# Kernel optimization log

Hardware: AMD Instinct MI355X
Metric: run time of the kernel (lower is better)

## Reference

```python
import jax, jax.numpy as jnp
import numpy as np
import math

# ---- HashGridEncoder constants (from init_kwargs) ----
L = 16            # levels
LOG2T = 19
T = 1 << LOG2T    # hash table size per level
F = 2             # features per entry
N_MIN = 16
N_MAX = 2048
N_PTS = 524288    # number of query points
BB_MIN = np.zeros(3, np.float32)
BB_MAX = np.ones(3, np.float32)
B = math.exp((math.log(N_MAX) - math.log(N_MIN)) / (L - 1))
RES = np.array([math.floor(N_MIN * B ** i) for i in range(L)], dtype=np.float32)  # per-level grid resolution
VERTS = np.array([[0,0,0],[0,0,1],[0,1,0],[0,1,1],[1,0,0],[1,0,1],[1,1,0],[1,1,1]], dtype=np.int32)  # 8 cube corners
PI = np.array([1, 2654435761, 805459861], dtype=np.uint32)  # spatial hash primes
MASK = np.uint32((1 << 19) - 1)  # hard-coded mask from source


def setup_inputs() -> dict:
    key = jax.random.key(0)
    k1, k2 = jax.random.split(key)
    xyz = jax.random.uniform(k1, (N_PTS, 3), dtype=jnp.float32)  # points inside bbox [0,1]^3
    # nn.init.uniform_(weight, -1e-4, 1e-4)
    tables = jax.random.uniform(k2, (L, T, F), minval=-1e-4, maxval=1e-4, dtype=jnp.float32)
    return {"xyz": xyz, "tables": tables}


def reference(xyz, tables):
    # cell size per level: (bb_max - bb_min) / resolution  -> [L,3]
    cell = (BB_MAX - BB_MIN)[None, :] / RES[:, None]
    # normalized grid coords for all levels at once: [L,N,3]
    u = (xyz[None, :, :] - BB_MIN) / cell[:, None, :]
    mi = jnp.floor(u).astype(jnp.int32)            # min corner index [L,N,3]
    d = u - mi.astype(jnp.float32)                 # trilinear fracs == (xyz - min_vertex)/cell, [L,N,3]
    # 8 corner integer coords: [L,N,8,3]; uint32 wrapping matches int64-mul + low-19-bit mask
    corners = (mi[:, :, None, :] + VERTS[None, None]).astype(jnp.uint32)
    h = (corners[..., 0] * PI[0]) ^ (corners[..., 1] * PI[1]) ^ (corners[..., 2] * PI[2])
    h = (h & MASK).astype(jnp.int32)               # hash indices [L,N,8], all < T
    # gather all levels in one flat lookup
    flat = tables.reshape(L * T, F)
    idx = h + (jnp.arange(L, dtype=jnp.int32) * T)[:, None, None]
    emb = flat[idx]                                # [L,N,8,F]
    # trilinear weights: prod over axes of d (corner bit 1) or 1-d (corner bit 0) -> [L,N,8]
    w = jnp.prod(jnp.where(VERTS[None, None].astype(bool), d[:, :, None, :], 1.0 - d[:, :, None, :]), axis=-1)
    c = jnp.einsum('lnv,lnvf->lnf', w, emb)        # interpolated features [L,N,F]
    # torch.cat(embedded, dim=-1): level-major concat -> [N, L*F]
    return jnp.moveaxis(c, 0, 1).reshape(xyz.shape[0], L * F)
```

## Files before the change

### kernel.cpp

```cpp
#include <hip/hip_runtime.h>
#include <cmath>

#define NLEVELS 16
#define HMASK   0x7FFFFu
#define NPTS    524288
#define NBUCKET 32768

typedef float v4f __attribute__((ext_vector_type(4)));
typedef float v2f __attribute__((ext_vector_type(2)));
typedef _Float16 h2 __attribute__((ext_vector_type(2)));

struct LevelParams {
    float cell[NLEVELS];
};

__device__ __forceinline__ unsigned spread5(unsigned v) {
    return (v & 1u) | ((v & 2u) << 2) | ((v & 4u) << 4) |
           ((v & 8u) << 6) | ((v & 16u) << 8);
}

__device__ __forceinline__ unsigned morton_key(float x, float y, float z) {
    unsigned bx = min(31u, (unsigned)(x * 32.0f));
    unsigned by = min(31u, (unsigned)(y * 32.0f));
    unsigned bz = min(31u, (unsigned)(z * 32.0f));
    return spread5(bx) | (spread5(by) << 1) | (spread5(bz) << 2);
}

__device__ __forceinline__ void ngp_hash(
    float x, float y, float z, float cell, unsigned* __restrict__ h,
    float& dx, float& dy, float& dz, unsigned& ix_out)
{
    const float ux = x / cell;
    const float uy = y / cell;
    const float uz = z / cell;
    const float fx = floorf(ux);
    const float fy = floorf(uy);
    const float fz = floorf(uz);
    dx = ux - fx;
    dy = uy - fy;
    dz = uz - fz;

    const unsigned ix = (unsigned)(int)fx;
    const unsigned iy = (unsigned)(int)fy;
    const unsigned iz = (unsigned)(int)fz;
    ix_out = ix;

    const unsigned hx0 = ix;
    const unsigned hx1 = ix + 1u;
    const unsigned hy0 = iy * 2654435761u;
    const unsigned hy1 = (iy + 1u) * 2654435761u;
    const unsigned hz0 = iz * 805459861u;
    const unsigned hz1 = (iz + 1u) * 805459861u;

    h[0] = (hx0 ^ hy0 ^ hz0) & HMASK;
    h[1] = (hx0 ^ hy0 ^ hz1) & HMASK;
    h[2] = (hx0 ^ hy1 ^ hz0) & HMASK;
    h[3] = (hx0 ^ hy1 ^ hz1) & HMASK;
    h[4] = (hx1 ^ hy0 ^ hz0) & HMASK;
    h[5] = (hx1 ^ hy0 ^ hz1) & HMASK;
    h[6] = (hx1 ^ hy1 ^ hz0) & HMASK;
    h[7] = (hx1 ^ hy1 ^ hz1) & HMASK;
}

__device__ __forceinline__ void ngp_weights(
    float dx, float dy, float dz, float* __restrict__ w)
{
    const float wx0 = 1.0f - dx;
    const float wy0 = 1.0f - dy;
    const float wz0 = 1.0f - dz;
    const float p00 = wx0 * wy0;
    const float p01 = wx0 * dy;
    const float p10 = dx * wy0;
    const float p11 = dx * dy;
    w[0] = p00 * wz0;
    w[1] = p00 * dz;
    w[2] = p01 * wz0;
    w[3] = p01 * dz;
    w[4] = p10 * wz0;
    w[5] = p10 * dz;
    w[6] = p11 * wz0;
    w[7] = p11 * dz;
}

__device__ __forceinline__ v2f ngp_combine(
    const float* __restrict__ w, const v2f* __restrict__ e)
{
    float c0 = w[0] * e[0].x;
    float c1 = w[0] * e[0].y;
    #pragma unroll
    for (int c = 1; c < 8; ++c) {
        c0 += w[c] * e[c].x;
        c1 += w[c] * e[c].y;
    }
    v2f r = { c0, c1 };
    return r;
}

__global__ __launch_bounds__(256) void bucket_count(
    const float* __restrict__ xyz, unsigned* __restrict__ counts)
{
    const int n = blockIdx.x * 256 + threadIdx.x;
    const float x = xyz[3 * n + 0];
    const float y = xyz[3 * n + 1];
    const float z = xyz[3 * n + 2];
    atomicAdd(&counts[morton_key(x, y, z)], 1u);
}

__global__ __launch_bounds__(1024) void bucket_scan(
    const unsigned* __restrict__ counts, unsigned* __restrict__ cursor)
{
    __shared__ unsigned c[NBUCKET];
    __shared__ unsigned wsum[16];
    const unsigned t = threadIdx.x;
    const unsigned lane = t & 63u;
    const unsigned wid = t >> 6;

    #pragma unroll
    for (int i = 0; i < 32; ++i) {
        const unsigned idx = (unsigned)i * 1024u + t;
        c[idx ^ ((idx >> 5) & 31u)] = counts[idx];
    }
    __syncthreads();

    unsigned s = 0;
    #pragma unroll
    for (int i = 0; i < 32; ++i) {
        const unsigned idx = t * 32u + (unsigned)i;
        s += c[idx ^ ((idx >> 5) & 31u)];
    }

    unsigned v = s;
    #pragma unroll
    for (unsigned off = 1; off < 64; off <<= 1) {
        const unsigned u = __shfl_up(v, off);
        if (lane >= off) v += u;
    }
    if (lane == 63u) wsum[wid] = v;
    __syncthreads();

    unsigned woff = 0;
    #pragma unroll
    for (unsigned w = 0; w < 16; ++w)
        woff += (w < wid) ? wsum[w] : 0u;

    unsigned excl = woff + (v - s);
    #pragma unroll
    for (int i = 0; i < 32; ++i) {
        const unsigned idx = t * 32u + (unsigned)i;
        const unsigned sw  = idx ^ ((idx >> 5) & 31u);
        const unsigned tmp = c[sw];
        c[sw] = excl;
        excl += tmp;
    }
    __syncthreads();

    #pragma unroll
    for (int i = 0; i < 32; ++i) {
        const unsigned idx = (unsigned)i * 1024u + t;
        cursor[idx] = c[idx ^ ((idx >> 5) & 31u)];
    }
}

__global__ __launch_bounds__(256) void bucket_scatter(
    const float* __restrict__ xyz, unsigned* __restrict__ cursor,
    v4f* __restrict__ pts)
{
    const int n = blockIdx.x * 256 + threadIdx.x;
    const float x = xyz[3 * n + 0];
    const float y = xyz[3 * n + 1];
    const float z = xyz[3 * n + 2];
    const unsigned key = morton_key(x, y, z);
    const unsigned p = atomicAdd(&cursor[key], 1u);
    v4f v = { x, y, z, __uint_as_float((unsigned)n) };
    __builtin_nontemporal_store(v, &pts[p]);
}

__global__ __launch_bounds__(256) void ngp_phase1(
    const v4f* __restrict__ pts,
    const float* __restrict__ tables,
    h2* __restrict__ ws,
    LevelParams lp)
{
    const unsigned b = blockIdx.x;
    const int level = (int)(b >> 11);
    const int chunk = (int)(b & 2047u);
    const int p = chunk * 256 + threadIdx.x;

    const v4f q = pts[p];

    const float cell = lp.cell[level];
    const v2f* __restrict__ tab = (const v2f*)tables + ((size_t)level << 19);

    unsigned h[8];
    float dx, dy, dz;
    unsigned ix;
    ngp_hash(q.x, q.y, q.z, cell, h, dx, dy, dz, ix);

    v2f e[8];
    if (!(ix & 1u)) {
        if (level >= 5) {
            v4f p0, p1, p2, p3;
            const v4f* a0 = (const v4f*)(tab + (h[0] & ~1u));
            const v4f* a1 = (const v4f*)(tab + (h[1] & ~1u));
            const v4f* a2 = (const v4f*)(tab + (h[2] & ~1u));
            const v4f* a3 = (const v4f*)(tab + (h[3] & ~1u));
            asm volatile(
                "global_load_dwordx4 %0, %4, off sc0\n\t"
                "global_load_dwordx4 %1, %5, off sc0\n\t"
                "global_load_dwordx4 %2, %6, off sc0\n\t"
                "global_load_dwordx4 %3, %7, off sc0"
                : "=&v"(p0), "=&v"(p1), "=&v"(p2), "=&v"(p3)
                : "v"(a0), "v"(a1), "v"(a2), "v"(a3));
            asm volatile(
                "s_waitcnt vmcnt(0)"
                : "+v"(p0), "+v"(p1), "+v"(p2), "+v"(p3));
            const bool o0 = (h[0] & 1u) != 0u;
            const bool o1 = (h[1] & 1u) != 0u;
            const bool o2 = (h[2] & 1u) != 0u;
            const bool o3 = (h[3] & 1u) != 0u;
            e[0].x = o0 ? p0.z : p0.x;  e[0].y = o0 ? p0.w : p0.y;
            e[4].x = o0 ? p0.x : p0.z;  e[4].y = o0 ? p0.y : p0.w;
            e[1].x = o1 ? p1.z : p1.x;  e[1].y = o1 ? p1.w : p1.y;
            e[5].x = o1 ? p1.x : p1.z;  e[5].y = o1 ? p1.y : p1.w;
            e[2].x = o2 ? p2.z : p2.x;  e[2].y = o2 ? p2.w : p2.y;
            e[6].x = o2 ? p2.x : p2.z;  e[6].y = o2 ? p2.y : p2.w;
            e[3].x = o3 ? p3.z : p3.x;  e[3].y = o3 ? p3.w : p3.y;
            e[7].x = o3 ? p3.x : p3.z;  e[7].y = o3 ? p3.y : p3.w;
        } else {
            #pragma unroll
            for (int c = 0; c < 4; ++c) {
                const v4f pv = *(const v4f*)(tab + (h[c] & ~1u));
                const bool o = (h[c] & 1u) != 0u;
                e[c].x     = o ? pv.z : pv.x;  e[c].y     = o ? pv.w : pv.y;
                e[c + 4].x = o ? pv.x : pv.z;  e[c + 4].y = o ? pv.y : pv.w;
            }
        }
    } else {
        if (level >= 5) {
            v2f e0, e1, e2, e3, e4, e5, e6, e7;
            asm volatile(
                "global_load_dwordx2 %0, %8, off sc0\n\t"
                "global_load_dwordx2 %1, %9, off sc0\n\t"
                "global_load_dwordx2 %2, %10, off sc0\n\t"
                "global_load_dwordx2 %3, %11, off sc0\n\t"
                "global_load_dwordx2 %4, %12, off sc0\n\t"
                "global_load_dwordx2 %5, %13, off sc0\n\t"
                "global_load_dwordx2 %6, %14, off sc0\n\t"
                "global_load_dwordx2 %7, %15, off sc0"
                : "=&v"(e0), "=&v"(e1), "=&v"(e2), "=&v"(e3),
                  "=&v"(e4), "=&v"(e5), "=&v"(e6), "=&v"(e7)
                : "v"(tab + h[0]), "v"(tab + h[1]), "v"(tab + h[2]), "v"(tab + h[3]),
                  "v"(tab + h[4]), "v"(tab + h[5]), "v"(tab + h[6]), "v"(tab + h[7]));
            asm volatile(
                "s_waitcnt vmcnt(0)"
                : "+v"(e0), "+v"(e1), "+v"(e2), "+v"(e3),
                  "+v"(e4), "+v"(e5), "+v"(e6), "+v"(e7));
            e[0] = e0; e[1] = e1; e[2] = e2; e[3] = e3;
            e[4] = e4; e[5] = e5; e[6] = e6; e[7] = e7;
        } else {
            #pragma unroll
            for (int c = 0; c < 8; ++c) e[c] = tab[h[c]];
        }
    }

    float w[8];
    ngp_weights(dx, dy, dz, w);

    const v2f r2 = ngp_combine(w, e);

    h2 hv = { (_Float16)r2.x, (_Float16)r2.y };
    __builtin_nontemporal_store(hv, &ws[(size_t)level * NPTS + p]);
}

#define P2S 258

__global__ __launch_bounds__(256) void ngp_phase2(
    const h2* __restrict__ ws,
    const v4f* __restrict__ pts,
    float* __restrict__ out)
{
    __shared__ h2 lds[NLEVELS * P2S];
    __shared__ unsigned nperm[256];
    const unsigned base = blockIdx.x * 256;
    const unsigned t = threadIdx.x;

    nperm[t] = __float_as_uint(pts[base + t].w);
    #pragma unroll
    for (int l = 0; l < NLEVELS; ++l)
        lds[l * P2S + t] =
            __builtin_nontemporal_load(&ws[(size_t)l * NPTS + base + t]);

    __syncthreads();

    #pragma unroll
    for (int it = 0; it < 8; ++it) {
        const unsigned j = it * 256 + t;
        const unsigned pl = j >> 3;
        const unsigned k = j & 7u;
        const h2 a = lds[(2u * k)      * P2S + pl];
        const h2 b = lds[(2u * k + 1u) * P2S + pl];
        v4f v = { (float)a.x, (float)a.y, (float)b.x, (float)b.y };
        __builtin_nontemporal_store(
            v, (v4f*)(out + (size_t)nperm[pl] * 32 + k * 4));
    }
}

__global__ __launch_bounds__(256) void ngp_encode(
    const float* __restrict__ xyz,
    const float* __restrict__ tables,
    float* __restrict__ out,
    LevelParams lp)
{
    const int n = blockIdx.x * 256 + threadIdx.x;
    const float x = xyz[3 * n + 0];
    const float y = xyz[3 * n + 1];
    const float z = xyz[3 * n + 2];

    float acc[2 * NLEVELS];
    const v2f* __restrict__ tab_base = (const v2f*)tables;

    #pragma unroll
    for (int l = 0; l < NLEVELS; ++l) {
        unsigned h[8];
        float dx, dy, dz;
        unsigned ix;
        ngp_hash(x, y, z, lp.cell[l], h, dx, dy, dz, ix);
        const v2f* __restrict__ tab = tab_base + ((size_t)l << 19);
        v2f e[8];
        #pragma unroll
        for (int c = 0; c < 8; ++c) e[c] = tab[h[c]];
        float w[8];
        ngp_weights(dx, dy, dz, w);
        const v2f r = ngp_combine(w, e);
        acc[2 * l + 0] = r.x;
        acc[2 * l + 1] = r.y;
    }

    v4f* o4 = (v4f*)(out + (size_t)n * 32);
    #pragma unroll
    for (int j = 0; j < 8; ++j) {
        v4f v = { acc[4 * j + 0], acc[4 * j + 1],
                  acc[4 * j + 2], acc[4 * j + 3] };
        o4[j] = v;
    }
}

extern "C" void kernel_launch(void* const* d_in, const int* in_sizes, int n_in,
                              void* d_out, int out_size, void* d_ws, size_t ws_size,
                              hipStream_t stream) {
    const float* xyz    = (const float*)d_in[0];
    const float* tables = (const float*)d_in[1];
    float* out          = (float*)d_out;

    LevelParams lp;
    const double B = std::exp((std::log(2048.0) - std::log(16.0)) / 15.0);
    for (int i = 0; i < NLEVELS; ++i) {
        const double r = std::floor(16.0 * std::pow(B, (double)i));
        lp.cell[i] = 1.0f / (float)r;
    }

    const size_t off_feat   = 0;
    const size_t off_pts    = off_feat + (size_t)NLEVELS * NPTS * sizeof(h2);
    const size_t off_counts = off_pts + (size_t)NPTS * sizeof(v4f);
    const size_t off_cursor = off_counts + (size_t)NBUCKET * sizeof(unsigned);
    const size_t ws_needed  = off_cursor + (size_t)NBUCKET * sizeof(unsigned);

    if (ws_size >= ws_needed) {
        char* wsb = (char*)d_ws;
        h2*       ws_feat = (h2*)(wsb + off_feat);
        v4f*      pts     = (v4f*)(wsb + off_pts);
        unsigned* counts  = (unsigned*)(wsb + off_counts);
        unsigned* cursor  = (unsigned*)(wsb + off_cursor);

        hipMemsetAsync(counts, 0, NBUCKET * sizeof(unsigned), stream);
        hipLaunchKernelGGL(bucket_count, dim3(NPTS / 256), dim3(256), 0, stream,
                           xyz, counts);
        hipLaunchKernelGGL(bucket_scan, dim3(1), dim3(1024), 0, stream,
                           counts, cursor);
        hipLaunchKernelGGL(bucket_scatter, dim3(NPTS / 256), dim3(256), 0, stream,
                           xyz, cursor, pts);
        hipLaunchKernelGGL(ngp_phase1, dim3(NLEVELS * (NPTS / 256)), dim3(256), 0, stream,
                           pts, tables, ws_feat, lp);
        hipLaunchKernelGGL(ngp_phase2, dim3(NPTS / 256), dim3(256), 0, stream,
                           ws_feat, pts, out);
    } else {
        hipLaunchKernelGGL(ngp_encode, dim3(NPTS / 256), dim3(256), 0, stream,
                           xyz, tables, out, lp);
    }
}
```

Baseline: 324.2 us.

## Replace single-block bucket scan with two-pass multi-block scan

The 32768-bucket exclusive prefix scan ran in a single 1024-thread block. It is now split into two kernels across 128 blocks. The first computes per-block totals, and the second has each block reduce the preceding block totals and then do an in-block scan. This aims to remove the serial single-CU scan step from the pipeline, at the cost of one extra kernel launch and a small extra workspace buffer.

```diff
diff --git a/kernel.cpp b/kernel.cpp
--- a/kernel.cpp
+++ b/kernel.cpp
@@ -106,59 +106,53 @@
     atomicAdd(&counts[morton_key(x, y, z)], 1u);
 }
 
-__global__ __launch_bounds__(1024) void bucket_scan(
-    const unsigned* __restrict__ counts, unsigned* __restrict__ cursor)
-{
-    __shared__ unsigned c[NBUCKET];
-    __shared__ unsigned wsum[16];
+__global__ __launch_bounds__(256) void scan_pre(
+    const unsigned* __restrict__ counts, unsigned* __restrict__ btot)
+{
+    __shared__ unsigned ws4[4];
+    const unsigned j = blockIdx.x;
+    const unsigned t = threadIdx.x;
+    unsigned v = counts[j * 256u + t];
+    #pragma unroll
+    for (unsigned off = 1; off < 64; off <<= 1) v += __shfl_xor(v, off);
+    if ((t & 63u) == 0u) ws4[t >> 6] = v;
+    __syncthreads();
+    if (t == 0u) btot[j] = ws4[0] + ws4[1] + ws4[2] + ws4[3];
+}
+
+__global__ __launch_bounds__(256) void scan_main(
+    const unsigned* __restrict__ counts, const unsigned* __restrict__ btot,
+    unsigned* __restrict__ cursor)
+{
+    __shared__ unsigned bsum4[4];
+    __shared__ unsigned wsum4[4];
+    const unsigned j = blockIdx.x;
     const unsigned t = threadIdx.x;
     const unsigned lane = t & 63u;
     const unsigned wid = t >> 6;
 
-    #pragma unroll
-    for (int i = 0; i < 32; ++i) {
-        const unsigned idx = (unsigned)i * 1024u + t;
-        c[idx ^ ((idx >> 5) & 31u)] = counts[idx];
-    }
+    unsigned bv = (t < j) ? btot[t] : 0u;
+    #pragma unroll
+    for (unsigned off = 1; off < 64; off <<= 1) bv += __shfl_xor(bv, off);
+    if (lane == 0u) bsum4[wid] = bv;
     __syncthreads();
-
-    unsigned s = 0;
-    #pragma unroll
-    for (int i = 0; i < 32; ++i) {
-        const unsigned idx = t * 32u + (unsigned)i;
-        s += c[idx ^ ((idx >> 5) & 31u)];
-    }
-
-    unsigned v = s;
+    const unsigned base = bsum4[0] + bsum4[1] + bsum4[2] + bsum4[3];
+
+    const unsigned idx = j * 256u + t;
+    const unsigned v = counts[idx];
+    unsigned incl = v;
     #pragma unroll
     for (unsigned off = 1; off < 64; off <<= 1) {
-        const unsigned u = __shfl_up(v, off);
-        if (lane >= off) v += u;
-    }
-    if (lane == 63u) wsum[wid] = v;
+        const unsigned u = __shfl_up(incl, off);
+        if (lane >= off) incl += u;
+    }
+    if (lane == 63u) wsum4[wid] = incl;
     __syncthreads();
-
     unsigned woff = 0;
     #pragma unroll
-    for (unsigned w = 0; w < 16; ++w)
-        woff += (w < wid) ? wsum[w] : 0u;
-
-    unsigned excl = woff + (v - s);
-    #pragma unroll
-    for (int i = 0; i < 32; ++i) {
-        const unsigned idx = t * 32u + (unsigned)i;
-        const unsigned sw  = idx ^ ((idx >> 5) & 31u);
-        const unsigned tmp = c[sw];
-        c[sw] = excl;
-        excl += tmp;
-    }
-    __syncthreads();
-
-    #pragma unroll
-    for (int i = 0; i < 32; ++i) {
-        const unsigned idx = (unsigned)i * 1024u + t;
-        cursor[idx] = c[idx ^ ((idx >> 5) & 31u)];
-    }
+    for (unsigned w = 0; w < 4; ++w) woff += (w < wid) ? wsum4[w] : 0u;
+
+    cursor[idx] = base + woff + incl - v;
 }
 
 __global__ __launch_bounds__(256) void bucket_scatter(
@@ -363,7 +357,8 @@
     const size_t off_pts    = off_feat + (size_t)NLEVELS * NPTS * sizeof(h2);
     const size_t off_counts = off_pts + (size_t)NPTS * sizeof(v4f);
     const size_t off_cursor = off_counts + (size_t)NBUCKET * sizeof(unsigned);
-    const size_t ws_needed  = off_cursor + (size_t)NBUCKET * sizeof(unsigned);
+    const size_t off_btot   = off_cursor + (size_t)NBUCKET * sizeof(unsigned);
+    const size_t ws_needed  = off_btot + 128 * sizeof(unsigned);
 
     if (ws_size >= ws_needed) {
         char* wsb = (char*)d_ws;
@@ -371,12 +366,15 @@
         v4f*      pts     = (v4f*)(wsb + off_pts);
         unsigned* counts  = (unsigned*)(wsb + off_counts);
         unsigned* cursor  = (unsigned*)(wsb + off_cursor);
+        unsigned* btot    = (unsigned*)(wsb + off_btot);
 
         hipMemsetAsync(counts, 0, NBUCKET * sizeof(unsigned), stream);
         hipLaunchKernelGGL(bucket_count, dim3(NPTS / 256), dim3(256), 0, stream,
                            xyz, counts);
-        hipLaunchKernelGGL(bucket_scan, dim3(1), dim3(1024), 0, stream,
-                           counts, cursor);
+        hipLaunchKernelGGL(scan_pre, dim3(NBUCKET / 256), dim3(256), 0, stream,
+                           counts, btot);
+        hipLaunchKernelGGL(scan_main, dim3(NBUCKET / 256), dim3(256), 0, stream,
+                           counts, btot, cursor);
         hipLaunchKernelGGL(bucket_scatter, dim3(NPTS / 256), dim3(256), 0, stream,
                            xyz, cursor, pts);
         hipLaunchKernelGGL(ngp_phase1, dim3(NLEVELS * (NPTS / 256)), dim3(256), 0, stream,
```

Result: no change. 324.6 us (+0.1%).
